# Optimization experiments

Measured on AMD Instinct MI355X. Metric: run time of the kernel, lower is better.

The kernel has to match this reference:

```python
import jax, jax.numpy as jnp
import numpy as np

BN_EPS = 1e-5
NORM_EPS = 1e-12  # F.normalize default eps


def _l2norm(v, axis):
    n = jnp.sqrt(jnp.sum(v * v, axis=axis, keepdims=True))
    return v / jnp.maximum(n, NORM_EPS)


def setup_inputs() -> dict:
    key = jax.random.key(0)
    ks = jax.random.split(key, 8)
    b, n_f, c, h, w = 2, 5, 256, 64, 64
    ck, cv = c // 8, c // 2
    x = jax.random.normal(ks[0], (b, n_f, c, h, w), dtype=jnp.float32)
    prev_mask = jax.random.uniform(ks[1], (b, n_f - 1, 1, h, w), dtype=jnp.float32)
    def xavier(k, shape):
        fan_out, fan_in = shape
        a = np.sqrt(6.0 / (fan_in + fan_out))
        return jax.random.uniform(k, shape, jnp.float32, -a, a)
    return {
        "x": x,
        "prev_mask": prev_mask,
        "qk_w": xavier(ks[2], (ck, c)),
        "qv_w": xavier(ks[3], (cv, c)),
        "mk_w": xavier(ks[4], (ck, c)),
        "mv_w": xavier(ks[5], (cv, c)),
        "sm_w": xavier(ks[6], (c, c)),
        "bn_scale": jnp.ones((c,), jnp.float32),
        "bn_bias": jnp.zeros((c,), jnp.float32),
        "bn_mean": jnp.zeros((c,), jnp.float32),
        "bn_var": jnp.ones((c,), jnp.float32),
    }


def reference(x, prev_mask, qk_w, qv_w, mk_w, mv_w, sm_w, bn_scale, bn_bias, bn_mean, bn_var):
    b, n_f, c, h, w = x.shape
    ck, cv = qk_w.shape[0], qv_w.shape[0]
    hw = h * w
    m = n_f - 1

    xq = x[:, -1]   # [b,c,h,w] query frame
    xm = x[:, :-1]  # [b,m,c,h,w] memory frames

    # 1x1 convs == channel matmuls
    query_k = jnp.einsum('bchw,oc->bohw', xq, qk_w)   # [b,ck,h,w]
    query_v = jnp.einsum('bchw,oc->bohw', xq, qv_w)   # [b,cv,h,w]
    mem_k = jnp.einsum('bmchw,oc->bmohw', xm, mk_w)   # [b,m,ck,h,w]
    mem_v = jnp.einsum('bmchw,oc->bmohw', xm, mv_w)   # [b,m,cv,h,w]

    qk = _l2norm(query_k.reshape(b, ck, hw), axis=1)          # [b,ck,hw]
    mk = _l2norm(mem_k.reshape(b, m * hw, ck)                 # note: [b,m,ck,hw]->[b,m,hw,ck] flatten
                 if False else
                 _reorder_mem_k(mem_k, b, m, ck, hw), axis=2)  # [b,m*hw,ck]

    # cosine-similarity attention over all memory pixels
    attn = jnp.einsum('bcq,bkc->bqk', qk, mk)                 # [b,hw,m*hw]
    attn = jax.nn.softmax(attn, axis=2)

    mv = mem_v.reshape(b, m, cv, hw).transpose(0, 1, 3, 2).reshape(b, m * hw, cv)
    agg = jnp.einsum('bqk,bkc->bqc', attn, mv)                # [b,hw,cv]
    agg = agg.transpose(0, 2, 1).reshape(b, cv, h, w)

    y = jnp.concatenate([query_v, agg], axis=1)               # [b,c,h,w]
    y = jnp.einsum('bchw,oc->bohw', y, sm_w)
    inv = bn_scale / jnp.sqrt(bn_var + BN_EPS)
    y = (y - bn_mean[None, :, None, None]) * inv[None, :, None, None] + bn_bias[None, :, None, None]
    y = jax.nn.relu(y)

    return jnp.concatenate([xm, y[:, None]], axis=1)          # [b,n_f,c,h,w]


def _reorder_mem_k(mem_k, b, m, ck, hw):
    # [b,m,ck,h,w] -> [b,m,ck,hw] -> [b,m,hw,ck] -> [b,m*hw,ck]
    return mem_k.reshape(b, m, ck, hw).transpose(0, 1, 3, 2).reshape(b, m * hw, ck)
```

## Files before the change

kernel.cpp:

```cpp
#include <hip/hip_runtime.h>

typedef unsigned short u16;
typedef unsigned int u32;
typedef __attribute__((ext_vector_type(8))) short short8v;
typedef __attribute__((ext_vector_type(4))) float f32x4;
typedef __attribute__((ext_vector_type(16))) float f32x16;
typedef __attribute__((ext_vector_type(2))) int i32x2;

#define B 2
#define NF 5
#define C 256
#define HW 4096
#define CV 128
#define NK 16384
#define NQ 4096

__device__ __forceinline__ u16 f2bf(float f) {
    u32 u = __float_as_uint(f);
    u32 r = (u + 0x7FFFu + ((u >> 16) & 1u)) >> 16;
    return (u16)r;
}

__device__ __forceinline__ u32 cvtpk(float lo, float hi) {
    u32 r;
    asm("v_cvt_pk_bf16_f32 %0, %1, %2" : "=v"(r) : "v"(lo), "v"(hi));
    return r;
}

__device__ __forceinline__ i32x2 plswap(u32 vdst, u32 src0) {
    return __builtin_amdgcn_permlane32_swap((int)vdst, (int)src0, false, false);
}

__global__ __launch_bounds__(256) void prep_k(
    const float* __restrict__ qk_w, const float* __restrict__ qv_w,
    const float* __restrict__ mk_w, const float* __restrict__ mv_w,
    const float* __restrict__ sm_w,
    const float* __restrict__ bns, const float* __restrict__ bnb,
    const float* __restrict__ bnm, const float* __restrict__ bnv,
    u16* __restrict__ wsf, float* __restrict__ bias2, u16* __restrict__ wb) {
    int bx = blockIdx.x, t = threadIdx.x;
    if (bx < 256) {
        int idx = bx * 256 + t;
        int o = idx >> 8;
        float inv = bns[o] / sqrtf(bnv[o] + 1e-5f);
        wsf[idx] = f2bf(sm_w[idx] * inv);
    } else if (bx < 576) {
        int j = (bx - 256) * 256 + t;
        int v = j / 40960, rr = j % 40960;
        int row = rr >> 8, c = rr & 255;
        float s;
        if (v == 0) s = (row < 32) ? mk_w[row * 256 + c] : mv_w[(row - 32) * 256 + c];
        else        s = (row < 32) ? qk_w[row * 256 + c] : qv_w[(row - 32) * 256 + c];
        wb[j] = f2bf(s);
    } else {
        int o = t;
        float inv = bns[o] / sqrtf(bnv[o] + 1e-5f);
        bias2[o] = bnb[o] - bnm[o] * inv;
    }
}

__global__ __launch_bounds__(256) void proj_mfma(
    const float* __restrict__ x, const u16* __restrict__ wb,
    u16* __restrict__ qkn, u16* __restrict__ mkn,
    u16* __restrict__ mvt, u16* __restrict__ U, float* __restrict__ out) {
    int bx = blockIdx.x;
    int bi = bx / 320;
    int rem = bx % 320;
    int f = rem >> 6, pt = rem & 63;
    int t = threadIdx.x, w = t >> 6, lane = t & 63;
    int l15 = lane & 15, cg = lane >> 4;
    int p = pt * 64 + w * 16 + l15;
    const float* xp = x + (((size_t)bi * NF + f) * C) * HW + p;
    const u16* wrow = wb + (size_t)((f == 4) ? 160 : 0) * 256;
    float* op = out + (((size_t)bi * NF + f) * C) * HW + p;

    f32x4 acc[10];
#pragma unroll
    for (int m = 0; m < 10; m++) acc[m] = (f32x4){0.f, 0.f, 0.f, 0.f};

    for (int k = 0; k < 8; k++) {
        float xv[8];
#pragma unroll
        for (int j = 0; j < 8; j++) xv[j] = xp[(size_t)(k * 32 + cg * 8 + j) * HW];
        if (f < 4) {
#pragma unroll
            for (int j = 0; j < 8; j++) op[(size_t)(k * 32 + cg * 8 + j) * HW] = xv[j];
        }
        short8v bfrag;
#pragma unroll
        for (int j = 0; j < 8; j++) bfrag[j] = (short)f2bf(xv[j]);
#pragma unroll
        for (int m = 0; m < 10; m++) {
            short8v afrag = *(const short8v*)(wrow + (size_t)(m * 16 + l15) * 256 + k * 32 + cg * 8);
            acc[m] = __builtin_amdgcn_mfma_f32_16x16x32_bf16(afrag, bfrag, acc[m], 0, 0, 0);
        }
    }

    float ssq = 0.f;
#pragma unroll
    for (int m = 0; m < 2; m++)
#pragma unroll
        for (int r = 0; r < 4; r++) ssq += acc[m][r] * acc[m][r];
    ssq += __shfl_xor(ssq, 16, 64);
    ssq += __shfl_xor(ssq, 32, 64);
    float rn = 1.0f / fmaxf(sqrtf(ssq), 1e-12f);

    if (f == 4) {
        float rq = rn * 1.44269504f;
        u16* kd = qkn + ((size_t)bi * NQ + p) * 32;
#pragma unroll
        for (int m = 0; m < 2; m++)
#pragma unroll
            for (int r = 0; r < 4; r++) kd[m * 16 + cg * 4 + r] = f2bf(acc[m][r] * rq);
        u16* ud = U + ((size_t)bi * HW + p) * 256;
#pragma unroll
        for (int m = 2; m < 10; m++) {
            int vo = m * 16 - 32 + cg * 4;
            union { u16 h[4]; uint2 v; } pk;
#pragma unroll
            for (int r = 0; r < 4; r++) pk.h[r] = f2bf(acc[m][r]);
            *(uint2*)(ud + vo) = pk.v;
        }
    } else {
        u16* kd = mkn + ((size_t)bi * NK + f * HW + p) * 32;
#pragma unroll
        for (int m = 0; m < 2; m++)
#pragma unroll
            for (int r = 0; r < 4; r++) kd[m * 16 + cg * 4 + r] = f2bf(acc[m][r] * rn);
#pragma unroll
        for (int m = 2; m < 10; m++)
#pragma unroll
            for (int r = 0; r < 4; r++) {
                int vo = m * 16 - 32 + cg * 4 + r;
                mvt[((size_t)bi * CV + vo) * NK + f * HW + p] = f2bf(acc[m][r]);
            }
    }
}

__global__ __launch_bounds__(256, 2) void attn_k(
    const u16* __restrict__ qkn, const u16* __restrict__ mkn,
    const u16* __restrict__ mvt, u16* __restrict__ opart,
    float* __restrict__ lpart, int kc) {
    __shared__ alignas(16) u16 kl[2][64 * 32];
    __shared__ alignas(16) u16 vl[2][128 * 64];

    int bx = blockIdx.x;
    int bi = bx / (32 * kc);
    int rem = bx % (32 * kc);
    int qt = rem / kc, kci = rem % kc;
    int chunk = NK / kc, iters = chunk / 64;
    int tid = threadIdx.x, w = tid >> 6, lane = tid & 63;
    int l31 = lane & 31, hi = lane >> 5;

    int qrow = qt * 128 + w * 32 + l31;
    const u16* qp = qkn + ((size_t)bi * NQ + qrow) * 32;
    short8v qf0 = *(const short8v*)(qp + hi * 8);
    short8v qf1 = *(const short8v*)(qp + 16 + hi * 8);

    f32x16 O[4];
#pragma unroll
    for (int n = 0; n < 4; n++)
#pragma unroll
        for (int i = 0; i < 16; i++) O[n][i] = 0.f;
    float ls[4] = {0.f, 0.f, 0.f, 0.f};

    const u16* mknb = mkn + (size_t)bi * NK * 32;
    const u16* mvtb = mvt + (size_t)bi * CV * NK;
    int krow = tid >> 2, kcol = tid & 3;
    int klsoff = krow * 32 + ((kcol ^ (krow & 3)) * 8);
    int vrow[4], vcol[4], vlsoff[4];
#pragma unroll
    for (int r = 0; r < 4; r++) {
        int cidx = tid + 256 * r;
        vrow[r] = cidx >> 3; vcol[r] = cidx & 7;
        vlsoff[r] = vrow[r] * 64 + ((vcol[r] ^ (vrow[r] & 7)) * 8);
    }

    const u16* kptr = mknb + (size_t)(kci * chunk + krow) * 32 + kcol * 8;
    const u16* vptr[4];
#pragma unroll
    for (int r = 0; r < 4; r++)
        vptr[r] = mvtb + (size_t)vrow[r] * NK + kci * chunk + vcol[r] * 8;

    short8v kreg = *(const short8v*)kptr;
    short8v vreg[4];
#pragma unroll
    for (int r = 0; r < 4; r++) vreg[r] = *(const short8v*)vptr[r];

    int c = 0;
    for (int it = 0; it < iters; ++it) {
        *(short8v*)(&kl[c][0] + klsoff) = kreg;
#pragma unroll
        for (int r = 0; r < 4; r++) *(short8v*)(&vl[c][0] + vlsoff[r]) = vreg[r];
        if (it + 1 < iters) {
            kptr += 64 * 32;
            kreg = *(const short8v*)kptr;
#pragma unroll
            for (int r = 0; r < 4; r++) {
                vptr[r] += 64;
                vreg[r] = *(const short8v*)vptr[r];
            }
        }
        __syncthreads();
        const u16* klr = &kl[c][0];
        const u16* vlr = &vl[c][0];
#pragma unroll
        for (int t = 0; t < 2; t++) {
            int ar = t * 32 + l31;
            const u16* kb = klr + ar * 32;
            short8v ka0 = *(const short8v*)(kb + ((hi ^ (ar & 3)) * 8));
            short8v ka1 = *(const short8v*)(kb + (((2 + hi) ^ (ar & 3)) * 8));
            f32x16 st;
#pragma unroll
            for (int i = 0; i < 16; i++) st[i] = 0.f;
            __builtin_amdgcn_s_setprio(1);
            st = __builtin_amdgcn_mfma_f32_32x32x16_bf16(ka0, qf0, st, 0, 0, 0);
            st = __builtin_amdgcn_mfma_f32_32x32x16_bf16(ka1, qf1, st, 0, 0, 0);
            __builtin_amdgcn_s_setprio(0);
            float p[16];
#pragma unroll
            for (int i = 0; i < 16; i++) p[i] = exp2f(st[i]);
#pragma unroll
            for (int g = 0; g < 4; g++)
                ls[g] += ((p[4 * g] + p[4 * g + 1]) + (p[4 * g + 2] + p[4 * g + 3]));
            u32 c0[4], c1[4];
#pragma unroll
            for (int g = 0; g < 4; g++) {
                c0[g] = cvtpk(p[4 * g], p[4 * g + 1]);
                c1[g] = cvtpk(p[4 * g + 2], p[4 * g + 3]);
            }
#pragma unroll
            for (int half = 0; half < 2; half++) {
                i32x2 s0 = plswap(c0[2 * half + 1], c0[2 * half]);
                i32x2 s1 = plswap(c1[2 * half + 1], c1[2 * half]);
                union { u32 wd[4]; short8v v; } bu;
                bu.wd[0] = (u32)s0[1];
                bu.wd[1] = (u32)s1[1];
                bu.wd[2] = (u32)s0[0];
                bu.wd[3] = (u32)s1[0];
                int kk = 2 * t + half;
                __builtin_amdgcn_s_setprio(1);
#pragma unroll
                for (int n = 0; n < 4; n++) {
                    int vr = n * 32 + l31;
                    short8v va = *(const short8v*)(vlr + vr * 64 + (((kk * 2 + hi) ^ (vr & 7)) * 8));
                    O[n] = __builtin_amdgcn_mfma_f32_32x32x16_bf16(va, bu.v, O[n], 0, 0, 0);
                }
                __builtin_amdgcn_s_setprio(0);
            }
        }
        c ^= 1;
    }

    float lsum = (ls[0] + ls[1]) + (ls[2] + ls[3]);
    lsum += __shfl_xor(lsum, 32, 64);
    uint2* op2 = (uint2*)opart;
    size_t pbase4 = (size_t)(bi * kc + kci) * 32;
#pragma unroll
    for (int n = 0; n < 4; n++)
#pragma unroll
        for (int g = 0; g < 4; g++) {
            uint2 val;
            val.x = cvtpk(O[n][4 * g + 0], O[n][4 * g + 1]);
            val.y = cvtpk(O[n][4 * g + 2], O[n][4 * g + 3]);
            int v4 = n * 8 + 2 * g + hi;
            op2[(pbase4 + v4) * NQ + qrow] = val;
        }
    if (hi == 0) lpart[(size_t)(bi * kc + kci) * NQ + qrow] = lsum;
}

__global__ __launch_bounds__(256) void combine_k(
    const u16* __restrict__ opart, const float* __restrict__ lpart,
    u16* __restrict__ U, int kc) {
    int bx = blockIdx.x;
    int bi = bx >> 7;
    int qb = ((bx >> 1) & 63) << 6;
    int vh = bx & 1;
    int t = threadIdx.x;
    int q = qb + (t & 63);
    int v40 = vh * 16 + (t >> 6) * 4;
    const uint2* op2 = (const uint2*)opart;
    float acc[16];
#pragma unroll
    for (int i = 0; i < 16; i++) acc[i] = 0.f;
    float lsum = 0.f;
    for (int k = 0; k < kc; k++) {
        size_t base4 = (size_t)(bi * kc + k) * 32 + v40;
#pragma unroll
        for (int j = 0; j < 4; j++) {
            uint2 d = op2[(base4 + j) * NQ + q];
            acc[4 * j + 0] += __uint_as_float(d.x << 16);
            acc[4 * j + 1] += __uint_as_float(d.x & 0xFFFF0000u);
            acc[4 * j + 2] += __uint_as_float(d.y << 16);
            acc[4 * j + 3] += __uint_as_float(d.y & 0xFFFF0000u);
        }
        lsum += lpart[(size_t)(bi * kc + k) * NQ + q];
    }
    float r = 1.0f / lsum;
    u16* ud = U + ((size_t)bi * HW + q) * 256 + 128 + v40 * 4;
    union { u16 h[8]; short8v v; } a, b;
#pragma unroll
    for (int e = 0; e < 8; e++) a.h[e] = f2bf(acc[e] * r);
#pragma unroll
    for (int e = 0; e < 8; e++) b.h[e] = f2bf(acc[8 + e] * r);
    *(short8v*)ud = a.v;
    *(short8v*)(ud + 8) = b.v;
}

__global__ __launch_bounds__(256) void final_mfma(
    const u16* __restrict__ U, const u16* __restrict__ wsf,
    const float* __restrict__ bias2, float* __restrict__ out) {
    int bx = blockIdx.x;
    int bi = bx >> 7;
    int mh = (bx >> 6) & 1;
    int pt = bx & 63;
    int t = threadIdx.x, w = t >> 6, lane = t & 63;
    int l15 = lane & 15, cg = lane >> 4;
    int p = pt * 64 + w * 16 + l15;
    const u16* urow = U + ((size_t)bi * HW + p) * 256;
    const u16* wbase = wsf + (size_t)mh * 128 * 256;
    f32x4 acc[8];
#pragma unroll
    for (int m = 0; m < 8; m++) acc[m] = (f32x4){0.f, 0.f, 0.f, 0.f};
    for (int k = 0; k < 8; k++) {
        short8v bfrag = *(const short8v*)(urow + k * 32 + cg * 8);
#pragma unroll
        for (int m = 0; m < 8; m++) {
            short8v afrag = *(const short8v*)(wbase + (size_t)(m * 16 + l15) * 256 + k * 32 + cg * 8);
            acc[m] = __builtin_amdgcn_mfma_f32_16x16x32_bf16(afrag, bfrag, acc[m], 0, 0, 0);
        }
    }
    float* obase = out + (((size_t)bi * NF + 4) * C) * HW;
#pragma unroll
    for (int m = 0; m < 8; m++) {
#pragma unroll
        for (int r = 0; r < 4; r++) {
            int o = mh * 128 + m * 16 + cg * 4 + r;
            obase[(size_t)o * HW + p] = fmaxf(acc[m][r] + bias2[o], 0.f);
        }
    }
}

extern "C" void kernel_launch(void* const* d_in, const int* in_sizes, int n_in,
                              void* d_out, int out_size, void* d_ws, size_t ws_size,
                              hipStream_t stream) {
    const float* x    = (const float*)d_in[0];
    const float* qk_w = (const float*)d_in[2];
    const float* qv_w = (const float*)d_in[3];
    const float* mk_w = (const float*)d_in[4];
    const float* mv_w = (const float*)d_in[5];
    const float* sm_w = (const float*)d_in[6];
    const float* bns  = (const float*)d_in[7];
    const float* bnb  = (const float*)d_in[8];
    const float* bnm  = (const float*)d_in[9];
    const float* bnv  = (const float*)d_in[10];
    float* out = (float*)d_out;
    char* ws = (char*)d_ws;

    size_t off = 0;
    auto alloc = [&](size_t bytes) { size_t o = off; off += (bytes + 255) & ~(size_t)255; return o; };
    size_t WSF = alloc(256 * 256 * 2);
    size_t BIA = alloc(256 * 4);
    size_t WB  = alloc(2 * 160 * 256 * 2);
    size_t QKN = alloc((size_t)B * NQ * 32 * 2);
    size_t MKN = alloc((size_t)B * NK * 32 * 2);
    size_t MVT = alloc((size_t)B * CV * NK * 2);
    size_t UBU = alloc((size_t)B * HW * 256 * 2);
    size_t fixed = off;
    int kc = 16;
    {
        auto need = [&](int k) {
            return fixed + (size_t)B * k * NQ * 4 + (size_t)B * k * (size_t)CV * NQ * 2 + 1024;
        };
        if (ws_size < need(16)) kc = (ws_size < need(8)) ? 4 : 8;
    }
    size_t LP = alloc((size_t)B * kc * NQ * 4);
    size_t OP = alloc((size_t)B * kc * (size_t)CV * NQ * 2);

    prep_k<<<577, 256, 0, stream>>>(qk_w, qv_w, mk_w, mv_w, sm_w, bns, bnb, bnm, bnv,
        (u16*)(ws + WSF), (float*)(ws + BIA), (u16*)(ws + WB));
    proj_mfma<<<640, 256, 0, stream>>>(x, (u16*)(ws + WB),
        (u16*)(ws + QKN), (u16*)(ws + MKN), (u16*)(ws + MVT), (u16*)(ws + UBU), out);
    attn_k<<<B * 32 * kc, 256, 0, stream>>>((u16*)(ws + QKN), (u16*)(ws + MKN),
        (u16*)(ws + MVT), (u16*)(ws + OP), (float*)(ws + LP), kc);
    combine_k<<<256, 256, 0, stream>>>((u16*)(ws + OP), (float*)(ws + LP),
        (u16*)(ws + UBU), kc);
    final_mfma<<<256, 256, 0, stream>>>((u16*)(ws + UBU), (u16*)(ws + WSF),
        (float*)(ws + BIA), out);
}
```

Measured before the change: 125.3 us.

## Load attention keys directly from global memory and pad V tile instead of swizzling

The attention kernel no longer stages memory keys through shared memory. Each lane now reads its key fragments straight from global memory inside the inner loop, which removes one LDS store, one LDS read pair and some address arithmetic per tile. The V tile layout switches from an XOR swizzle to a padded row stride of 72, and the launch-bounds occupancy hint is dropped. The direct key loads sit on the critical path before the QK MFMA with no prefetch, so global latency may stall the loop, and the workspace fallback no longer considers kc=4.

```diff
diff --git a/kernel.cpp b/kernel.cpp
--- a/kernel.cpp
+++ b/kernel.cpp
@@ -137,12 +137,11 @@
     }
 }
 
-__global__ __launch_bounds__(256, 2) void attn_k(
+__global__ __launch_bounds__(256) void attn_k(
     const u16* __restrict__ qkn, const u16* __restrict__ mkn,
     const u16* __restrict__ mvt, u16* __restrict__ opart,
     float* __restrict__ lpart, int kc) {
-    __shared__ alignas(16) u16 kl[2][64 * 32];
-    __shared__ alignas(16) u16 vl[2][128 * 64];
+    __shared__ alignas(16) u16 vl[2][128 * 72];
 
     int bx = blockIdx.x;
     int bi = bx / (32 * kc);
@@ -163,38 +162,36 @@
 #pragma unroll
         for (int i = 0; i < 16; i++) O[n][i] = 0.f;
     float ls[4] = {0.f, 0.f, 0.f, 0.f};
+    f32x16 kz;
+#pragma unroll
+    for (int i = 0; i < 16; i++) kz[i] = 0.f;
 
     const u16* mknb = mkn + (size_t)bi * NK * 32;
     const u16* mvtb = mvt + (size_t)bi * CV * NK;
-    int krow = tid >> 2, kcol = tid & 3;
-    int klsoff = krow * 32 + ((kcol ^ (krow & 3)) * 8);
+    const u16* kg = mknb + ((size_t)kci * chunk + l31) * 32 + hi * 8;
+
     int vrow[4], vcol[4], vlsoff[4];
 #pragma unroll
     for (int r = 0; r < 4; r++) {
         int cidx = tid + 256 * r;
         vrow[r] = cidx >> 3; vcol[r] = cidx & 7;
-        vlsoff[r] = vrow[r] * 64 + ((vcol[r] ^ (vrow[r] & 7)) * 8);
-    }
-
-    const u16* kptr = mknb + (size_t)(kci * chunk + krow) * 32 + kcol * 8;
+        vlsoff[r] = vrow[r] * 72 + vcol[r] * 8;
+    }
+
     const u16* vptr[4];
 #pragma unroll
     for (int r = 0; r < 4; r++)
         vptr[r] = mvtb + (size_t)vrow[r] * NK + kci * chunk + vcol[r] * 8;
 
-    short8v kreg = *(const short8v*)kptr;
     short8v vreg[4];
 #pragma unroll
     for (int r = 0; r < 4; r++) vreg[r] = *(const short8v*)vptr[r];
 
     int c = 0;
     for (int it = 0; it < iters; ++it) {
-        *(short8v*)(&kl[c][0] + klsoff) = kreg;
 #pragma unroll
         for (int r = 0; r < 4; r++) *(short8v*)(&vl[c][0] + vlsoff[r]) = vreg[r];
         if (it + 1 < iters) {
-            kptr += 64 * 32;
-            kreg = *(const short8v*)kptr;
 #pragma unroll
             for (int r = 0; r < 4; r++) {
                 vptr[r] += 64;
@@ -202,19 +199,14 @@
             }
         }
         __syncthreads();
-        const u16* klr = &kl[c][0];
         const u16* vlr = &vl[c][0];
 #pragma unroll
         for (int t = 0; t < 2; t++) {
-            int ar = t * 32 + l31;
-            const u16* kb = klr + ar * 32;
-            short8v ka0 = *(const short8v*)(kb + ((hi ^ (ar & 3)) * 8));
-            short8v ka1 = *(const short8v*)(kb + (((2 + hi) ^ (ar & 3)) * 8));
-            f32x16 st;
-#pragma unroll
-            for (int i = 0; i < 16; i++) st[i] = 0.f;
+            const u16* kgp = kg + (size_t)(it * 64 + t * 32) * 32;
+            short8v ka0 = *(const short8v*)kgp;
+            short8v ka1 = *(const short8v*)(kgp + 16);
             __builtin_amdgcn_s_setprio(1);
-            st = __builtin_amdgcn_mfma_f32_32x32x16_bf16(ka0, qf0, st, 0, 0, 0);
+            f32x16 st = __builtin_amdgcn_mfma_f32_32x32x16_bf16(ka0, qf0, kz, 0, 0, 0);
             st = __builtin_amdgcn_mfma_f32_32x32x16_bf16(ka1, qf1, st, 0, 0, 0);
             __builtin_amdgcn_s_setprio(0);
             float p[16];
@@ -243,7 +235,7 @@
 #pragma unroll
                 for (int n = 0; n < 4; n++) {
                     int vr = n * 32 + l31;
-                    short8v va = *(const short8v*)(vlr + vr * 64 + (((kk * 2 + hi) ^ (vr & 7)) * 8));
+                    short8v va = *(const short8v*)(vlr + vr * 72 + (kk * 2 + hi) * 8);
                     O[n] = __builtin_amdgcn_mfma_f32_32x32x16_bf16(va, bu.v, O[n], 0, 0, 0);
                 }
                 __builtin_amdgcn_s_setprio(0);
@@ -372,7 +364,7 @@
         auto need = [&](int k) {
             return fixed + (size_t)B * k * NQ * 4 + (size_t)B * k * (size_t)CV * NQ * 2 + 1024;
         };
-        if (ws_size < need(16)) kc = (ws_size < need(8)) ? 4 : 8;
+        if (ws_size < need(16)) kc = 8;
     }
     size_t LP = alloc((size_t)B * kc * NQ * 4);
     size_t OP = alloc((size_t)B * kc * (size_t)CV * NQ * 2);
```

Measured after the change: 133.2 us. 1.06x slower.
